# Kernel optimization log

Hardware: AMD Instinct MI355X
Metric: run time of the kernel (lower is better)

Reference implementation:

```python
import jax, jax.numpy as jnp
import numpy as np

NUM_HEAD = 8
D_MODEL = 512
HEAD_DIM = D_MODEL // NUM_HEAD
SCALING = HEAD_DIM ** (-0.5)
B, NQ, NK = 2, 2048, 2048


def setup_inputs() -> dict:
    key = jax.random.key(0)
    ks = jax.random.split(key, 12)
    s = 1.0 / np.sqrt(D_MODEL)
    return {
        "q": jax.random.normal(ks[0], (B, NQ, D_MODEL), jnp.float32),
        "k": jax.random.normal(ks[1], (B, NK, D_MODEL), jnp.float32),
        "v": jax.random.normal(ks[2], (B, NK, D_MODEL), jnp.float32),
        "mask_head": jax.random.uniform(ks[3], (B, NUM_HEAD, NQ, NK), jnp.float32),
        "pearson_matrix": jax.random.normal(ks[4], (B, NUM_HEAD, NK, NK), jnp.float32),
        "Wq": jax.random.uniform(ks[5], (D_MODEL, D_MODEL), jnp.float32, -s, s),
        "bq": jax.random.uniform(ks[6], (D_MODEL,), jnp.float32, -s, s),
        "Wk": jax.random.uniform(ks[7], (D_MODEL, D_MODEL), jnp.float32, -s, s),
        "bk": jax.random.uniform(ks[8], (D_MODEL,), jnp.float32, -s, s),
        "Wv": jax.random.uniform(ks[9], (D_MODEL, D_MODEL), jnp.float32, -s, s),
        "bv": jax.random.uniform(ks[10], (D_MODEL,), jnp.float32, -s, s),
    }


def _split_heads(x):
    b, n, _ = x.shape
    return x.reshape(b, n, NUM_HEAD, HEAD_DIM).transpose(0, 2, 1, 3)  # b h n d


def reference(q, k, v, mask_head, pearson_matrix, Wq, bq, Wk, bk, Wv, bv):
    queries = _split_heads(q @ Wq.T + bq)
    keys = _split_heads(k @ Wk.T + bk)
    values = _split_heads(v @ Wv.T + bv)
    energy = jnp.einsum('bhqd,bhkd->bhqk', queries, keys) * SCALING
    att = jax.nn.softmax(energy, axis=-1)
    att = att * mask_head
    # einsum 'bhqk,bhkk->bhqk' = multiply by diagonal of pearson over last two axes
    diag = jnp.diagonal(pearson_matrix, axis1=-2, axis2=-1)  # b h k
    att = att * diag[:, :, None, :]
    agg = jnp.einsum('bhqk,bhkd->bhqd', att, values)
    b, h, n, d = agg.shape
    return agg.transpose(0, 2, 1, 3).reshape(b, n, h * d)
```

## Files before the change

### kernel.cpp

```cpp
#include <hip/hip_runtime.h>

#define NUM_HEAD 8
#define D_MODEL  512
#define HEAD_DIM 64
#define NSEQ     2048
#define SCALE_LOG2E 0.18033688011112042f

typedef __attribute__((ext_vector_type(8))) short bf16x8;
typedef __attribute__((ext_vector_type(4))) float f32x4;
typedef __attribute__((ext_vector_type(4))) float vf4;

static __device__ __forceinline__ unsigned short f2bf(float f) {
    unsigned u = __builtin_bit_cast(unsigned, f);
    u += 0x7fffu + ((u >> 16) & 1u);
    return (unsigned short)(u >> 16);
}
static __device__ __forceinline__ float bf2f(unsigned short h) {
    unsigned u = ((unsigned)h) << 16;
    return __builtin_bit_cast(float, u);
}
static __device__ __forceinline__ unsigned pk2(float a, float b) {
    return (unsigned)f2bf(a) | ((unsigned)f2bf(b) << 16);
}

#define PSTR 40

__global__ __launch_bounds__(256) void proj3_kernel(
    const float* __restrict__ Xq, const float* __restrict__ Xk, const float* __restrict__ Xv,
    const float* __restrict__ Wq, const float* __restrict__ Wk, const float* __restrict__ Wv,
    const float* __restrict__ bq, const float* __restrict__ bk, const float* __restrict__ bv,
    unsigned short* __restrict__ Qp, unsigned short* __restrict__ Kp,
    unsigned short* __restrict__ Vt)
{
    __shared__ unsigned short lA[128 * PSTR];
    __shared__ unsigned short lB[64 * PSTR];

    const int z = blockIdx.z;
    const float* X    = (z == 0) ? Xq : (z == 1) ? Xk : Xv;
    const float* W    = (z == 0) ? Wq : (z == 1) ? Wk : Wv;
    const float* bias = (z == 0) ? bq : (z == 1) ? bk : bv;

    const int tid  = threadIdx.x;
    const int lane = tid & 63, wid = tid >> 6;
    const int quad = lane >> 4, l15 = lane & 15;
    const int wm = (wid >> 1) * 64;
    const int wn = (wid & 1) * 32;
    const int m0 = blockIdx.x * 128, n0 = blockIdx.y * 64;

    f32x4 acc[4][2];
    const f32x4 zf = {0.f, 0.f, 0.f, 0.f};
#pragma unroll
    for (int mi = 0; mi < 4; mi++)
#pragma unroll
        for (int ni = 0; ni < 2; ni++) acc[mi][ni] = zf;

    const int arow = tid >> 1, akc = (tid & 1) * 16;
    const int brow = tid >> 2, bkc = (tid & 3) * 8;

    for (int k0 = 0; k0 < D_MODEL; k0 += 32) {
        const float* ap = X + (m0 + arow) * D_MODEL + k0 + akc;
        float4 a0 = *(const float4*)(ap);
        float4 a1 = *(const float4*)(ap + 4);
        float4 a2 = *(const float4*)(ap + 8);
        float4 a3 = *(const float4*)(ap + 12);
        uint4 w0, w1;
        w0.x = pk2(a0.x, a0.y); w0.y = pk2(a0.z, a0.w);
        w0.z = pk2(a1.x, a1.y); w0.w = pk2(a1.z, a1.w);
        w1.x = pk2(a2.x, a2.y); w1.y = pk2(a2.z, a2.w);
        w1.z = pk2(a3.x, a3.y); w1.w = pk2(a3.z, a3.w);
        *(uint4*)&lA[arow * PSTR + akc]     = w0;
        *(uint4*)&lA[arow * PSTR + akc + 8] = w1;
        const float* bp = W + (n0 + brow) * D_MODEL + k0 + bkc;
        float4 b0 = *(const float4*)(bp);
        float4 b1 = *(const float4*)(bp + 4);
        uint4 wb;
        wb.x = pk2(b0.x, b0.y); wb.y = pk2(b0.z, b0.w);
        wb.z = pk2(b1.x, b1.y); wb.w = pk2(b1.z, b1.w);
        *(uint4*)&lB[brow * PSTR + bkc] = wb;
        __syncthreads();

        bf16x8 aF[4], bF[2];
#pragma unroll
        for (int mi = 0; mi < 4; mi++)
            aF[mi] = *(const bf16x8*)&lA[(wm + mi * 16 + l15) * PSTR + quad * 8];
#pragma unroll
        for (int ni = 0; ni < 2; ni++)
            bF[ni] = *(const bf16x8*)&lB[(wn + ni * 16 + l15) * PSTR + quad * 8];
#pragma unroll
        for (int mi = 0; mi < 4; mi++)
#pragma unroll
            for (int ni = 0; ni < 2; ni++)
                acc[mi][ni] = __builtin_amdgcn_mfma_f32_16x16x32_bf16(
                    aF[mi], bF[ni], acc[mi][ni], 0, 0, 0);
        __syncthreads();
    }

    const float oscale = (z == 0) ? SCALE_LOG2E : 1.0f;
    const float bv0 = bias[n0 + wn + l15];
    const float bv1 = bias[n0 + wn + 16 + l15];
    unsigned short* outp = (z == 0) ? Qp : Kp;
#pragma unroll
    for (int mi = 0; mi < 4; mi++) {
        const int mbase = m0 + wm + mi * 16 + quad * 4;
#pragma unroll
        for (int ni = 0; ni < 2; ni++) {
            const int c = n0 + wn + ni * 16 + l15;
            const int h = c >> 6, d = c & 63;
            const float bb_add = ni ? bv1 : bv0;
#pragma unroll
            for (int r = 0; r < 4; r++) {
                const int mm = mbase + r;
                const int bb = mm >> 11, n = mm & 2047;
                const float val = (acc[mi][ni][r] + bb_add) * oscale;
                if (z < 2)
                    outp[((bb * NUM_HEAD + h) * NSEQ + n) * HEAD_DIM + d] = f2bf(val);
                else
                    Vt[((bb * NUM_HEAD + h) * HEAD_DIM + d) * NSEQ + n] = f2bf(val);
            }
        }
    }
}

__global__ void diag_kernel(const float* __restrict__ pearson,
                            float* __restrict__ diag)
{
    const int t = blockIdx.x * blockDim.x + threadIdx.x;
    const int bh = t >> 11, kk = t & 2047;
    diag[t] = __builtin_nontemporal_load(
        pearson + ((size_t)(bh * NSEQ + kk)) * NSEQ + kk);
}

#define VSTR 68

__global__ __launch_bounds__(256) void attn_kernel(
    const unsigned short* __restrict__ Qp, const unsigned short* __restrict__ Kp,
    const unsigned short* __restrict__ Vt, const float* __restrict__ diag,
    const float* __restrict__ mask, float* __restrict__ out)
{
    __shared__ unsigned short lP[64 * VSTR];

    const int tid  = threadIdx.x;
    const int lane = tid & 63, wid = tid >> 6;
    const int quad = lane >> 4, l15 = lane & 15;
    const int bh = blockIdx.y;
    const int q0 = blockIdx.x * 64;

    const unsigned short* Qb  = Qp + (size_t)bh * NSEQ * HEAD_DIM;
    const unsigned short* Kb  = Kp + (size_t)bh * NSEQ * HEAD_DIM;
    const unsigned short* Vtb = Vt + (size_t)bh * HEAD_DIM * NSEQ;
    const float* mrow  = mask + (size_t)bh * NSEQ * NSEQ
                              + (size_t)(q0 + wid * 16 + l15) * NSEQ + quad * 8;
    const float* diagb = diag + bh * NSEQ + quad * 8;

    bf16x8 qF[2];
    {
        const unsigned short* qp = Qb + (q0 + wid * 16 + l15) * HEAD_DIM + quad * 8;
        qF[0] = *(const bf16x8*)qp;
        qF[1] = *(const bf16x8*)(qp + 32);
    }

    const f32x4 zf = {0.f, 0.f, 0.f, 0.f};
    f32x4 oacc[4] = {zf, zf, zf, zf};
    float lacc[4] = {0.f, 0.f, 0.f, 0.f};

    const int lpw = (wid * 16 + quad * 4) * VSTR + l15;
    const int lpr = (wid * 16 + l15) * VSTR + quad * 8;

    for (int kt = 0; kt < NSEQ; kt += 64) {
        bf16x8 kF[4][2];
#pragma unroll
        for (int nt = 0; nt < 4; nt++) {
            const unsigned short* kp = Kb + (kt + nt * 16 + l15) * HEAD_DIM + quad * 8;
            kF[nt][0] = *(const bf16x8*)kp;
            kF[nt][1] = *(const bf16x8*)(kp + 32);
        }
        bf16x8 vF[2][4];
#pragma unroll
        for (int ks = 0; ks < 2; ks++)
#pragma unroll
            for (int nt = 0; nt < 4; nt++)
                vF[ks][nt] = *(const bf16x8*)&Vtb[(nt * 16 + l15) * NSEQ
                                                  + kt + ks * 32 + quad * 8];
        vf4 mA[4], dA[4];
#pragma unroll
        for (int ks = 0; ks < 2; ks++) {
            mA[2 * ks]     = __builtin_nontemporal_load((const vf4*)(mrow + kt + ks * 32));
            mA[2 * ks + 1] = __builtin_nontemporal_load((const vf4*)(mrow + kt + ks * 32 + 4));
            dA[2 * ks]     = *(const vf4*)(diagb + kt + ks * 32);
            dA[2 * ks + 1] = *(const vf4*)(diagb + kt + ks * 32 + 4);
        }

        f32x4 sacc[4];
#pragma unroll
        for (int nt = 0; nt < 4; nt++) {
            sacc[nt] = __builtin_amdgcn_mfma_f32_16x16x32_bf16(qF[0], kF[nt][0], zf, 0, 0, 0);
            sacc[nt] = __builtin_amdgcn_mfma_f32_16x16x32_bf16(qF[1], kF[nt][1], sacc[nt], 0, 0, 0);
        }

#pragma unroll
        for (int cf = 0; cf < 4; cf++)
#pragma unroll
            for (int r = 0; r < 4; r++) {
                const float p = __builtin_amdgcn_exp2f(sacc[cf][r]);
                lacc[r] += p;
                lP[lpw + r * VSTR + cf * 16] = f2bf(p);
            }

#pragma unroll
        for (int ks = 0; ks < 2; ks++) {
            const bf16x8 aP = *(const bf16x8*)&lP[lpr + ks * 32];
            bf16x8 aM;
#pragma unroll
            for (int j = 0; j < 8; j++) {
                const float mj = (j < 4) ? mA[2 * ks][j] : mA[2 * ks + 1][j - 4];
                const float dj = (j < 4) ? dA[2 * ks][j] : dA[2 * ks + 1][j - 4];
                aM[j] = (short)f2bf(bf2f((unsigned short)aP[j]) * mj * dj);
            }
#pragma unroll
            for (int nt = 0; nt < 4; nt++)
                oacc[nt] = __builtin_amdgcn_mfma_f32_16x16x32_bf16(aM, vF[ks][nt], oacc[nt], 0, 0, 0);
        }
    }

#pragma unroll
    for (int r = 0; r < 4; r++) {
        float v = lacc[r];
        v += __shfl_xor(v, 1);
        v += __shfl_xor(v, 2);
        v += __shfl_xor(v, 4);
        v += __shfl_xor(v, 8);
        lacc[r] = v;
    }

    const int b = bh >> 3, h = bh & 7;
#pragma unroll
    for (int nt = 0; nt < 4; nt++)
#pragma unroll
        for (int r = 0; r < 4; r++) {
            const int qrow = q0 + wid * 16 + quad * 4 + r;
            __builtin_nontemporal_store(
                oacc[nt][r] / lacc[r],
                out + ((size_t)b * NSEQ + qrow) * D_MODEL + h * HEAD_DIM + nt * 16 + l15);
        }
}

extern "C" void kernel_launch(void* const* d_in, const int* in_sizes, int n_in,
                              void* d_out, int out_size, void* d_ws, size_t ws_size,
                              hipStream_t stream) {
    const float* q       = (const float*)d_in[0];
    const float* k       = (const float*)d_in[1];
    const float* v       = (const float*)d_in[2];
    const float* mask    = (const float*)d_in[3];
    const float* pearson = (const float*)d_in[4];
    const float* Wq      = (const float*)d_in[5];
    const float* bq      = (const float*)d_in[6];
    const float* Wk      = (const float*)d_in[7];
    const float* bk      = (const float*)d_in[8];
    const float* Wv      = (const float*)d_in[9];
    const float* bv      = (const float*)d_in[10];

    unsigned short* Qp = (unsigned short*)d_ws;
    unsigned short* Kp = Qp + 2097152;
    unsigned short* Vtp = Kp + 2097152;
    float* diag = (float*)((char*)d_ws + 12582912);
    float* out = (float*)d_out;

    proj3_kernel<<<dim3(32, 8, 3), 256, 0, stream>>>(q, k, v, Wq, Wk, Wv,
                                                     bq, bk, bv, Qp, Kp, Vtp);
    diag_kernel<<<dim3(128), 256, 0, stream>>>(pearson, diag);
    attn_kernel<<<dim3(32, 16), 256, 0, stream>>>(Qp, Kp, Vtp, diag, mask, out);
}
```

Before: 655.7 us.

## Double-buffer K/V/mask register tiles in attention and widen projection K-step

The attention loop now software-pipelines its global loads. It prefetches the next 64-key tile of K, V and mask into a second register set while computing the current tile, which is meant to hide memory latency on the streaming mask reads. The projection GEMM now stages 64-wide K slices per barrier pair instead of 32, halving the number of syncs. Both kernels gain a launch_bounds minimum of 2 blocks per CU, which raises register pressure and risks spills. The last prefetch wraps around and reloads tile 0 redundantly.

Result: faster. 628.4 us (-4.2%).

```diff
diff --git a/kernel.cpp b/kernel.cpp
--- a/kernel.cpp
+++ b/kernel.cpp
@@ -23,9 +23,9 @@
     return (unsigned)f2bf(a) | ((unsigned)f2bf(b) << 16);
 }
 
-#define PSTR 40
-
-__global__ __launch_bounds__(256) void proj3_kernel(
+#define PSTR 72
+
+__global__ __launch_bounds__(256, 2) void proj3_kernel(
     const float* __restrict__ Xq, const float* __restrict__ Xk, const float* __restrict__ Xv,
     const float* __restrict__ Wq, const float* __restrict__ Wk, const float* __restrict__ Wv,
     const float* __restrict__ bq, const float* __restrict__ bk, const float* __restrict__ bv,
@@ -54,44 +54,55 @@
 #pragma unroll
         for (int ni = 0; ni < 2; ni++) acc[mi][ni] = zf;
 
-    const int arow = tid >> 1, akc = (tid & 1) * 16;
-    const int brow = tid >> 2, bkc = (tid & 3) * 8;
-
-    for (int k0 = 0; k0 < D_MODEL; k0 += 32) {
+    const int arow = tid >> 1, akc = (tid & 1) * 32;
+    const int brow = tid >> 2, bkc = (tid & 3) * 16;
+
+    for (int k0 = 0; k0 < D_MODEL; k0 += 64) {
         const float* ap = X + (m0 + arow) * D_MODEL + k0 + akc;
-        float4 a0 = *(const float4*)(ap);
-        float4 a1 = *(const float4*)(ap + 4);
-        float4 a2 = *(const float4*)(ap + 8);
-        float4 a3 = *(const float4*)(ap + 12);
-        uint4 w0, w1;
-        w0.x = pk2(a0.x, a0.y); w0.y = pk2(a0.z, a0.w);
-        w0.z = pk2(a1.x, a1.y); w0.w = pk2(a1.z, a1.w);
-        w1.x = pk2(a2.x, a2.y); w1.y = pk2(a2.z, a2.w);
-        w1.z = pk2(a3.x, a3.y); w1.w = pk2(a3.z, a3.w);
-        *(uint4*)&lA[arow * PSTR + akc]     = w0;
-        *(uint4*)&lA[arow * PSTR + akc + 8] = w1;
+        float4 av[8];
+#pragma unroll
+        for (int i = 0; i < 8; i++) av[i] = *(const float4*)(ap + 4 * i);
         const float* bp = W + (n0 + brow) * D_MODEL + k0 + bkc;
-        float4 b0 = *(const float4*)(bp);
-        float4 b1 = *(const float4*)(bp + 4);
-        uint4 wb;
-        wb.x = pk2(b0.x, b0.y); wb.y = pk2(b0.z, b0.w);
-        wb.z = pk2(b1.x, b1.y); wb.w = pk2(b1.z, b1.w);
-        *(uint4*)&lB[brow * PSTR + bkc] = wb;
+        float4 bvv[4];
+#pragma unroll
+        for (int i = 0; i < 4; i++) bvv[i] = *(const float4*)(bp + 4 * i);
+
+#pragma unroll
+        for (int i = 0; i < 4; i++) {
+            uint4 w;
+            w.x = pk2(av[2 * i].x, av[2 * i].y);
+            w.y = pk2(av[2 * i].z, av[2 * i].w);
+            w.z = pk2(av[2 * i + 1].x, av[2 * i + 1].y);
+            w.w = pk2(av[2 * i + 1].z, av[2 * i + 1].w);
+            *(uint4*)&lA[arow * PSTR + akc + 8 * i] = w;
+        }
+#pragma unroll
+        for (int i = 0; i < 2; i++) {
+            uint4 w;
+            w.x = pk2(bvv[2 * i].x, bvv[2 * i].y);
+            w.y = pk2(bvv[2 * i].z, bvv[2 * i].w);
+            w.z = pk2(bvv[2 * i + 1].x, bvv[2 * i + 1].y);
+            w.w = pk2(bvv[2 * i + 1].z, bvv[2 * i + 1].w);
+            *(uint4*)&lB[brow * PSTR + bkc + 8 * i] = w;
+        }
         __syncthreads();
 
-        bf16x8 aF[4], bF[2];
-#pragma unroll
-        for (int mi = 0; mi < 4; mi++)
-            aF[mi] = *(const bf16x8*)&lA[(wm + mi * 16 + l15) * PSTR + quad * 8];
-#pragma unroll
-        for (int ni = 0; ni < 2; ni++)
-            bF[ni] = *(const bf16x8*)&lB[(wn + ni * 16 + l15) * PSTR + quad * 8];
-#pragma unroll
-        for (int mi = 0; mi < 4; mi++)
+#pragma unroll
+        for (int ks = 0; ks < 2; ks++) {
+            bf16x8 aF[4], bF[2];
+#pragma unroll
+            for (int mi = 0; mi < 4; mi++)
+                aF[mi] = *(const bf16x8*)&lA[(wm + mi * 16 + l15) * PSTR + ks * 32 + quad * 8];
 #pragma unroll
             for (int ni = 0; ni < 2; ni++)
-                acc[mi][ni] = __builtin_amdgcn_mfma_f32_16x16x32_bf16(
-                    aF[mi], bF[ni], acc[mi][ni], 0, 0, 0);
+                bF[ni] = *(const bf16x8*)&lB[(wn + ni * 16 + l15) * PSTR + ks * 32 + quad * 8];
+#pragma unroll
+            for (int mi = 0; mi < 4; mi++)
+#pragma unroll
+                for (int ni = 0; ni < 2; ni++)
+                    acc[mi][ni] = __builtin_amdgcn_mfma_f32_16x16x32_bf16(
+                        aF[mi], bF[ni], acc[mi][ni], 0, 0, 0);
+        }
         __syncthreads();
     }
 
@@ -132,7 +143,77 @@
 
 #define VSTR 68
 
-__global__ __launch_bounds__(256) void attn_kernel(
+__device__ __forceinline__ void load_tile(
+    const unsigned short* __restrict__ Kb, const unsigned short* __restrict__ Vtb,
+    const float* __restrict__ mrow, int kt, int l15, int quad,
+    bf16x8 (&kF)[4][2], bf16x8 (&vF)[2][4], vf4 (&mA)[4])
+{
+#pragma unroll
+    for (int nt = 0; nt < 4; nt++) {
+        const unsigned short* kp = Kb + (kt + nt * 16 + l15) * HEAD_DIM + quad * 8;
+        kF[nt][0] = *(const bf16x8*)kp;
+        kF[nt][1] = *(const bf16x8*)(kp + 32);
+    }
+#pragma unroll
+    for (int ks = 0; ks < 2; ks++)
+#pragma unroll
+        for (int nt = 0; nt < 4; nt++)
+            vF[ks][nt] = *(const bf16x8*)&Vtb[(nt * 16 + l15) * NSEQ
+                                              + kt + ks * 32 + quad * 8];
+#pragma unroll
+    for (int ks = 0; ks < 2; ks++) {
+        mA[2 * ks]     = __builtin_nontemporal_load((const vf4*)(mrow + kt + ks * 32));
+        mA[2 * ks + 1] = __builtin_nontemporal_load((const vf4*)(mrow + kt + ks * 32 + 4));
+    }
+}
+
+__device__ __forceinline__ void compute_tile(
+    const bf16x8 (&qF)[2], const bf16x8 (&kF)[4][2], const bf16x8 (&vF)[2][4],
+    const vf4 (&mA)[4], const float* __restrict__ diagb, int kt,
+    unsigned short* lP, int lpw, int lpr,
+    f32x4 (&oacc)[4], float (&lacc)[4])
+{
+    const f32x4 zf = {0.f, 0.f, 0.f, 0.f};
+    vf4 dA[4];
+#pragma unroll
+    for (int ks = 0; ks < 2; ks++) {
+        dA[2 * ks]     = *(const vf4*)(diagb + kt + ks * 32);
+        dA[2 * ks + 1] = *(const vf4*)(diagb + kt + ks * 32 + 4);
+    }
+
+    f32x4 sacc[4];
+#pragma unroll
+    for (int nt = 0; nt < 4; nt++) {
+        sacc[nt] = __builtin_amdgcn_mfma_f32_16x16x32_bf16(qF[0], kF[nt][0], zf, 0, 0, 0);
+        sacc[nt] = __builtin_amdgcn_mfma_f32_16x16x32_bf16(qF[1], kF[nt][1], sacc[nt], 0, 0, 0);
+    }
+
+#pragma unroll
+    for (int cf = 0; cf < 4; cf++)
+#pragma unroll
+        for (int r = 0; r < 4; r++) {
+            const float p = __builtin_amdgcn_exp2f(sacc[cf][r]);
+            lacc[r] += p;
+            lP[lpw + r * VSTR + cf * 16] = f2bf(p);
+        }
+
+#pragma unroll
+    for (int ks = 0; ks < 2; ks++) {
+        const bf16x8 aP = *(const bf16x8*)&lP[lpr + ks * 32];
+        bf16x8 aM;
+#pragma unroll
+        for (int j = 0; j < 8; j++) {
+            const float mj = (j < 4) ? mA[2 * ks][j] : mA[2 * ks + 1][j - 4];
+            const float dj = (j < 4) ? dA[2 * ks][j] : dA[2 * ks + 1][j - 4];
+            aM[j] = (short)f2bf(bf2f((unsigned short)aP[j]) * mj * dj);
+        }
+#pragma unroll
+        for (int nt = 0; nt < 4; nt++)
+            oacc[nt] = __builtin_amdgcn_mfma_f32_16x16x32_bf16(aM, vF[ks][nt], oacc[nt], 0, 0, 0);
+    }
+}
+
+__global__ __launch_bounds__(256, 2) void attn_kernel(
     const unsigned short* __restrict__ Qp, const unsigned short* __restrict__ Kp,
     const unsigned short* __restrict__ Vt, const float* __restrict__ diag,
     const float* __restrict__ mask, float* __restrict__ out)
@@ -166,60 +247,18 @@
     const int lpw = (wid * 16 + quad * 4) * VSTR + l15;
     const int lpr = (wid * 16 + l15) * VSTR + quad * 8;
 
-    for (int kt = 0; kt < NSEQ; kt += 64) {
-        bf16x8 kF[4][2];
-#pragma unroll
-        for (int nt = 0; nt < 4; nt++) {
-            const unsigned short* kp = Kb + (kt + nt * 16 + l15) * HEAD_DIM + quad * 8;
-            kF[nt][0] = *(const bf16x8*)kp;
-            kF[nt][1] = *(const bf16x8*)(kp + 32);
-        }
-        bf16x8 vF[2][4];
-#pragma unroll
-        for (int ks = 0; ks < 2; ks++)
-#pragma unroll
-            for (int nt = 0; nt < 4; nt++)
-                vF[ks][nt] = *(const bf16x8*)&Vtb[(nt * 16 + l15) * NSEQ
-                                                  + kt + ks * 32 + quad * 8];
-        vf4 mA[4], dA[4];
-#pragma unroll
-        for (int ks = 0; ks < 2; ks++) {
-            mA[2 * ks]     = __builtin_nontemporal_load((const vf4*)(mrow + kt + ks * 32));
-            mA[2 * ks + 1] = __builtin_nontemporal_load((const vf4*)(mrow + kt + ks * 32 + 4));
-            dA[2 * ks]     = *(const vf4*)(diagb + kt + ks * 32);
-            dA[2 * ks + 1] = *(const vf4*)(diagb + kt + ks * 32 + 4);
-        }
-
-        f32x4 sacc[4];
-#pragma unroll
-        for (int nt = 0; nt < 4; nt++) {
-            sacc[nt] = __builtin_amdgcn_mfma_f32_16x16x32_bf16(qF[0], kF[nt][0], zf, 0, 0, 0);
-            sacc[nt] = __builtin_amdgcn_mfma_f32_16x16x32_bf16(qF[1], kF[nt][1], sacc[nt], 0, 0, 0);
-        }
-
-#pragma unroll
-        for (int cf = 0; cf < 4; cf++)
-#pragma unroll
-            for (int r = 0; r < 4; r++) {
-                const float p = __builtin_amdgcn_exp2f(sacc[cf][r]);
-                lacc[r] += p;
-                lP[lpw + r * VSTR + cf * 16] = f2bf(p);
-            }
-
-#pragma unroll
-        for (int ks = 0; ks < 2; ks++) {
-            const bf16x8 aP = *(const bf16x8*)&lP[lpr + ks * 32];
-            bf16x8 aM;
-#pragma unroll
-            for (int j = 0; j < 8; j++) {
-                const float mj = (j < 4) ? mA[2 * ks][j] : mA[2 * ks + 1][j - 4];
-                const float dj = (j < 4) ? dA[2 * ks][j] : dA[2 * ks + 1][j - 4];
-                aM[j] = (short)f2bf(bf2f((unsigned short)aP[j]) * mj * dj);
-            }
-#pragma unroll
-            for (int nt = 0; nt < 4; nt++)
-                oacc[nt] = __builtin_amdgcn_mfma_f32_16x16x32_bf16(aM, vF[ks][nt], oacc[nt], 0, 0, 0);
-        }
+    bf16x8 kF0[4][2], kF1[4][2];
+    bf16x8 vF0[2][4], vF1[2][4];
+    vf4 mA0[4], mA1[4];
+
+    load_tile(Kb, Vtb, mrow, 0, l15, quad, kF0, vF0, mA0);
+
+    for (int kt = 0; kt < NSEQ; kt += 128) {
+        load_tile(Kb, Vtb, mrow, kt + 64, l15, quad, kF1, vF1, mA1);
+        compute_tile(qF, kF0, vF0, mA0, diagb, kt, lP, lpw, lpr, oacc, lacc);
+        const int ktn = (kt + 128) & (NSEQ - 1);
+        load_tile(Kb, Vtb, mrow, ktn, l15, quad, kF0, vF0, mA0);
+        compute_tile(qF, kF1, vF1, mA1, diagb, kt + 64, lP, lpw, lpr, oacc, lacc);
     }
 
 #pragma unroll
```
